# Kernel tuning notes

Measured on AMD Instinct MI355X. Metric: run time of the kernel, lower is better.

Reference implementation:

```python
import jax, jax.numpy as jnp
import numpy as np

Z, N, D_MODEL, HEADS = 2, 2048, 1024, 16
DK = D_MODEL // HEADS


def setup_inputs() -> dict:
    key = jax.random.key(0)
    ks = jax.random.split(key, 9)
    xavier = (6.0 / (DK + D_MODEL)) ** 0.5
    x = jax.random.normal(ks[0], (Z, N, D_MODEL), jnp.float32)
    mask = jax.random.randint(ks[1], (Z, N), 0, 2) > 0  # bool validity mask
    q_proj = jax.random.uniform(ks[2], (HEADS, D_MODEL, DK), jnp.float32, -xavier, xavier)
    k_proj = jax.random.uniform(ks[3], (HEADS, D_MODEL, DK), jnp.float32, -xavier, xavier)
    v_proj = jax.random.uniform(ks[4], (HEADS, D_MODEL, DK), jnp.float32, -xavier, xavier)
    q_bias = jnp.zeros((HEADS, DK), jnp.float32)
    k_bias = jnp.zeros((HEADS, DK), jnp.float32)
    v_bias = jnp.zeros((HEADS, DK), jnp.float32)
    lim = 1.0 / (D_MODEL ** 0.5)
    out_w = jax.random.uniform(ks[5], (D_MODEL, D_MODEL), jnp.float32, -lim, lim)  # torch Linear weight [out, in]
    return {"x": x, "mask": mask, "q_proj": q_proj, "k_proj": k_proj, "v_proj": v_proj,
            "q_bias": q_bias, "k_bias": k_bias, "v_bias": v_bias, "out_w": out_w}


def reference(x, mask, q_proj, k_proj, v_proj, q_bias, k_bias, v_bias, out_w):
    # Per-head QKV projections: [Z,N,Dm] x [H,Dm,Dk] -> [Z,H,N,Dk]
    Q = jnp.einsum('znd,hdk->zhnk', x, q_proj) + q_bias[None, :, None, :]
    K = jnp.einsum('znd,hdk->zhnk', x, k_proj) + k_bias[None, :, None, :]
    V = jnp.einsum('znd,hdk->zhnk', x, v_proj) + v_bias[None, :, None, :]
    scale = q_proj.shape[-1] ** -0.5
    # Dense equivalent of flash_attn_varlen over valid (unpadded) tokens:
    # mask invalid keys, softmax, then zero outputs at invalid query positions.
    scores = jnp.einsum('zhnk,zhmk->zhnm', Q, K) * scale
    neg = jnp.asarray(-1e9, scores.dtype)
    scores = jnp.where(mask[:, None, None, :], scores, neg)
    attn = jax.nn.softmax(scores, axis=-1)
    ctx = jnp.einsum('zhnm,zhmk->zhnk', attn, V)
    ctx = jnp.where(mask[:, None, :, None], ctx, jnp.zeros((), ctx.dtype))
    z, h, n, dk = ctx.shape
    out = ctx.transpose(0, 2, 1, 3).reshape(z, n, h * dk)  # [Z,N,Dm]
    return out @ out_w.T  # nn.Linear(d_model, d_model, bias=False)
```

## Files before the change

### kernel.cpp

```cpp
#include <hip/hip_runtime.h>
#include <stdint.h>

typedef __bf16 bf16_t;
typedef __bf16 bf16x8 __attribute__((ext_vector_type(8)));
typedef __bf16 bf16x4 __attribute__((ext_vector_type(4)));
typedef float f32x4 __attribute__((ext_vector_type(4)));

#define MFMA16(A, B, C) __builtin_amdgcn_mfma_f32_16x16x32_bf16(A, B, C, 0, 0, 0)

#if __has_builtin(__builtin_amdgcn_exp2f)
#define EXP2F(x) __builtin_amdgcn_exp2f(x)
#else
#define EXP2F(x) exp2f(x)
#endif

#define GLOAD_LDS16(g, l)                                                   \
  __builtin_amdgcn_global_load_lds(                                         \
      (const __attribute__((address_space(1))) void*)(g),                   \
      (__attribute__((address_space(3))) void*)(l), 16, 0, 0)

#define SL2E 0.18033688011112042f
#define VT_STRIDE 131072

__global__ __launch_bounds__(256) void convert_kernel(
    const float* __restrict__ x, const float* __restrict__ qw, const float* __restrict__ kw,
    const float* __restrict__ vw, const float* __restrict__ qb, const float* __restrict__ kb,
    const float* __restrict__ vb, const float* __restrict__ ow,
    bf16_t* __restrict__ xb, bf16_t* __restrict__ wqkv, bf16_t* __restrict__ wo,
    float* __restrict__ bias)
{
  const int64_t TOT = 4194304LL + 3145728LL + 1048576LL + 3072LL;
  for (int64_t idx = (int64_t)blockIdx.x * blockDim.x + threadIdx.x; idx < TOT;
       idx += (int64_t)gridDim.x * blockDim.x) {
    if (idx < 4194304) {
      xb[idx] = (bf16_t)x[idx];
    } else if (idx < 4194304 + 3145728) {
      int j = (int)(idx - 4194304);
      int nn = j >> 10, d = j & 1023;
      int sec = nn >> 10, hk = nn & 1023;
      int h = hk >> 6, k = hk & 63;
      const float* w = sec == 0 ? qw : (sec == 1 ? kw : vw);
      wqkv[j] = (bf16_t)w[(h * 1024 + d) * 64 + k];
    } else if (idx < 4194304 + 3145728 + 1048576) {
      int j = (int)(idx - (4194304 + 3145728));
      wo[j] = (bf16_t)ow[j];
    } else {
      int j = (int)(idx - (4194304 + 3145728 + 1048576));
      int sec = j >> 10, c = j & 1023;
      const float* b = sec == 0 ? qb : (sec == 1 ? kb : vb);
      bias[j] = b[c];
    }
  }
}

template <int MODE, int TM>
__global__ __launch_bounds__(256) void gemm_kernel(
    const bf16_t* __restrict__ A, const bf16_t* __restrict__ Bt, const float* __restrict__ bias,
    bf16_t* __restrict__ qout, bf16_t* __restrict__ kout, bf16_t* __restrict__ vtout,
    float* __restrict__ fout, int Ndim)
{
  const int Kdim = 1024;
  const int MT = TM / 32;
  __shared__ bf16_t As[TM * 64];
  __shared__ bf16_t Bs[128 * 64];
  const int tid = threadIdx.x;
  const int wave = tid >> 6, lane = tid & 63;
  const int l15 = lane & 15, quad = lane >> 4;
  const int wr = wave >> 1, wc = wave & 1;
  const int nb = Ndim >> 7;
  const int bm = (blockIdx.x / nb) * TM;
  const int bn = (blockIdx.x % nb) * 128;

  f32x4 acc[MT][4] = {};

  const int lr = lane >> 3;
  const int lc = (lane & 7) * 8;

  for (int kk = 0; kk < Kdim; kk += 64) {
    __syncthreads();
#pragma unroll
    for (int j = 0; j < MT; j++) {
      int r = wave * (TM / 4) + j * 8;
      GLOAD_LDS16(A + (int64_t)(bm + r + lr) * Kdim + kk + lc, &As[r * 64]);
    }
#pragma unroll
    for (int j = 0; j < 4; j++) {
      int r = wave * 32 + j * 8;
      GLOAD_LDS16(Bt + (int64_t)(bn + r + lr) * Kdim + kk + lc, &Bs[r * 64]);
    }
    __syncthreads();
#pragma unroll
    for (int kc = 0; kc < 2; kc++) {
      bf16x8 af[MT], bfr[4];
#pragma unroll
      for (int mt = 0; mt < MT; mt++)
        af[mt] = *(const bf16x8*)&As[(wr * (TM / 2) + mt * 16 + l15) * 64 + kc * 32 + quad * 8];
#pragma unroll
      for (int nt = 0; nt < 4; nt++)
        bfr[nt] = *(const bf16x8*)&Bs[(wc * 64 + nt * 16 + l15) * 64 + kc * 32 + quad * 8];
#pragma unroll
      for (int mt = 0; mt < MT; mt++)
#pragma unroll
        for (int nt = 0; nt < 4; nt++) acc[mt][nt] = MFMA16(af[mt], bfr[nt], acc[mt][nt]);
    }
  }

#pragma unroll
  for (int mt = 0; mt < MT; mt++) {
#pragma unroll
    for (int nt = 0; nt < 4; nt++) {
#pragma unroll
      for (int r = 0; r < 4; r++) {
        int row = bm + wr * (TM / 2) + mt * 16 + quad * 4 + r;
        int col = bn + wc * 64 + nt * 16 + l15;
        float v = acc[mt][nt][r];
        if (MODE == 0) {
          v += bias[col];
          int sec = col >> 10, hk = col & 1023;
          int hh = hk >> 6, dk = hk & 63;
          int z = row >> 11, n = row & 2047;
          int zh = z * 16 + hh;
          if (sec == 0) {
            qout[(((int64_t)zh * 2048 + n) << 6) + dk] = (bf16_t)(v * SL2E);
          } else if (sec == 1) {
            kout[(((int64_t)zh * 2048 + n) << 6) + dk] = (bf16_t)v;
          } else {
            vtout[(int64_t)zh * VT_STRIDE + dk * 2048 + n] = (bf16_t)v;
          }
        } else {
          fout[(int64_t)row * Ndim + col] = v;
        }
      }
    }
  }
}

__global__ __launch_bounds__(256, 2) void attn_kernel(
    const bf16_t* __restrict__ Q, const bf16_t* __restrict__ K, const bf16_t* __restrict__ Vt,
    const int* __restrict__ mask, bf16_t* __restrict__ ctx)
{
  __shared__ bf16_t Ks[2][64 * 72];
  __shared__ bf16_t Vs[2][64 * 72];
  __shared__ float Mkf[2048];
  __shared__ bf16_t Ps[4][32 * 72];

  const int tid = threadIdx.x;
  const int wave = tid >> 6, lane = tid & 63;
  const int l15 = lane & 15, quad = lane >> 4;
  const int bid = blockIdx.x;
  const int qt = bid & 15, zh = bid >> 4;
  const int z = zh >> 4, h = zh & 15;

  const bf16_t* Qb = Q + ((int64_t)zh * 2048 + qt * 128) * 64;
  const bf16_t* Kb = K + (int64_t)zh * 2048 * 64;
  const bf16_t* Vb = Vt + (int64_t)zh * VT_STRIDE;
  bf16_t* Psw = Ps[wave];

  const int srow = lane >> 3;
  const int scol = (lane & 7) * 8;

  bf16x8 qf[2][2];
#pragma unroll
  for (int s = 0; s < 2; s++) {
    qf[s][0] = *(const bf16x8*)&Qb[(wave * 32 + s * 16 + l15) * 64 + quad * 8];
    qf[s][1] = *(const bf16x8*)&Qb[(wave * 32 + s * 16 + l15) * 64 + 32 + quad * 8];
  }

  {
    const int4* mp = (const int4*)(mask + z * 2048);
    for (int i = tid; i < 512; i += 256) {
      int4 m4 = mp[i];
      float4 f;
      f.x = m4.x ? 0.f : -1e30f;
      f.y = m4.y ? 0.f : -1e30f;
      f.z = m4.z ? 0.f : -1e30f;
      f.w = m4.w ? 0.f : -1e30f;
      *(float4*)&Mkf[i * 4] = f;
    }
  }

  {
    uint4 kp[2], vp[2];
#pragma unroll
    for (int j = 0; j < 2; j++) {
      int r = wave * 16 + j * 8 + srow;
      kp[j] = *(const uint4*)&Kb[(int64_t)r * 64 + scol];
      vp[j] = *(const uint4*)&Vb[(int64_t)r * 2048 + scol];
    }
#pragma unroll
    for (int j = 0; j < 2; j++) {
      int r = wave * 16 + j * 8 + srow;
      *(uint4*)&Ks[0][r * 72 + scol] = kp[j];
      *(uint4*)&Vs[0][r * 72 + scol] = vp[j];
    }
  }
  __syncthreads();

  float l_run[2] = {0.f, 0.f};
  f32x4 o[2][4] = {};
  int cur = 0;

  for (int kt = 0; kt < 32; kt++) {
    uint4 kp[2], vp[2];
    if (kt < 31) {
#pragma unroll
      for (int j = 0; j < 2; j++) {
        int r = wave * 16 + j * 8 + srow;
        kp[j] = *(const uint4*)&Kb[(int64_t)((kt + 1) * 64 + r) * 64 + scol];
        vp[j] = *(const uint4*)&Vb[(int64_t)r * 2048 + (kt + 1) * 64 + scol];
      }
    }

    f32x4 minit[4];
    bf16x8 kf0[4], kf1[4];
#pragma unroll
    for (int mb = 0; mb < 4; mb++) {
      minit[mb] = *(const f32x4*)&Mkf[kt * 64 + mb * 16 + quad * 4];
      kf0[mb] = *(const bf16x8*)&Ks[cur][(mb * 16 + l15) * 72 + quad * 8];
      kf1[mb] = *(const bf16x8*)&Ks[cur][(mb * 16 + l15) * 72 + 32 + quad * 8];
    }

#pragma unroll
    for (int s = 0; s < 2; s++) {
      float rs = 0.f;
#pragma unroll
      for (int mb = 0; mb < 4; mb++) {
        f32x4 t = minit[mb];
        t = MFMA16(kf0[mb], qf[s][0], t);
        t = MFMA16(kf1[mb], qf[s][1], t);
        bf16x4 pk;
#pragma unroll
        for (int r = 0; r < 4; r++) {
          float p = EXP2F(t[r]);
          rs += p;
          pk[r] = (bf16_t)p;
        }
        *(bf16x4*)&Psw[(s * 16 + l15) * 72 + mb * 16 + quad * 4] = pk;
      }
      l_run[s] += rs;
    }

    bf16x8 p0[2], p1[2];
#pragma unroll
    for (int s = 0; s < 2; s++) {
      p0[s] = *(const bf16x8*)&Psw[(s * 16 + l15) * 72 + quad * 8];
      p1[s] = *(const bf16x8*)&Psw[(s * 16 + l15) * 72 + 32 + quad * 8];
    }

#pragma unroll
    for (int nb = 0; nb < 4; nb++) {
      bf16x8 v0 = *(const bf16x8*)&Vs[cur][(nb * 16 + l15) * 72 + quad * 8];
      bf16x8 v1 = *(const bf16x8*)&Vs[cur][(nb * 16 + l15) * 72 + 32 + quad * 8];
#pragma unroll
      for (int s = 0; s < 2; s++) {
        o[s][nb] = MFMA16(p0[s], v0, o[s][nb]);
        o[s][nb] = MFMA16(p1[s], v1, o[s][nb]);
      }
    }

    if (kt < 31) {
#pragma unroll
      for (int j = 0; j < 2; j++) {
        int r = wave * 16 + j * 8 + srow;
        *(uint4*)&Ks[cur ^ 1][r * 72 + scol] = kp[j];
        *(uint4*)&Vs[cur ^ 1][r * 72 + scol] = vp[j];
      }
    }
    __syncthreads();
    cur ^= 1;
  }

#pragma unroll
  for (int s = 0; s < 2; s++) {
    float l = l_run[s];
    l += __shfl_xor(l, 16);
    l += __shfl_xor(l, 32);
    float inv4[4];
#pragma unroll
    for (int r = 0; r < 4; r++) {
      int qrow = qt * 128 + wave * 32 + s * 16 + quad * 4 + r;
      float lv = __shfl(l, quad * 4 + r);
      int valid = mask[z * 2048 + qrow];
      inv4[r] = (valid && lv > 0.f) ? 1.0f / lv : 0.f;
    }
#pragma unroll
    for (int nb = 0; nb < 4; nb++) {
#pragma unroll
      for (int r = 0; r < 4; r++) {
        int qrow = qt * 128 + wave * 32 + s * 16 + quad * 4 + r;
        ctx[((int64_t)(z * 2048 + qrow)) * 1024 + h * 64 + nb * 16 + l15] =
            (bf16_t)(o[s][nb][r] * inv4[r]);
      }
    }
  }
}

extern "C" void kernel_launch(void* const* d_in, const int* in_sizes, int n_in,
                              void* d_out, int out_size, void* d_ws, size_t ws_size,
                              hipStream_t stream)
{
  (void)in_sizes; (void)n_in; (void)out_size; (void)ws_size;
  const float* x  = (const float*)d_in[0];
  const int* mask = (const int*)d_in[1];
  const float* qw = (const float*)d_in[2];
  const float* kw = (const float*)d_in[3];
  const float* vw = (const float*)d_in[4];
  const float* qb = (const float*)d_in[5];
  const float* kb = (const float*)d_in[6];
  const float* vb = (const float*)d_in[7];
  const float* ow = (const float*)d_in[8];
  float* out = (float*)d_out;

  bf16_t* xb   = (bf16_t*)d_ws;
  bf16_t* wqkv = xb + 4194304;
  bf16_t* wo   = wqkv + 3145728;
  float*  bias = (float*)(wo + 1048576);
  bf16_t* Qb   = (bf16_t*)(bias + 3072);
  bf16_t* Kb   = Qb + 4194304;
  bf16_t* Vtb  = Kb + 4194304;
  bf16_t* ctx  = Vtb + (int64_t)32 * VT_STRIDE;

  convert_kernel<<<4096, 256, 0, stream>>>(x, qw, kw, vw, qb, kb, vb, ow,
                                           xb, wqkv, wo, bias);
  gemm_kernel<0, 128><<<(4096 / 128) * (3072 / 128), 256, 0, stream>>>(
      xb, wqkv, bias, Qb, Kb, Vtb, nullptr, 3072);
  attn_kernel<<<2 * 16 * 16, 256, 0, stream>>>(Qb, Kb, Vtb, mask, ctx);
  gemm_kernel<1, 64><<<(4096 / 64) * (1024 / 128), 256, 0, stream>>>(
      ctx, wo, nullptr, nullptr, nullptr, nullptr, out, 1024);
}
```

Measured before the change: 238.3 us.

## Vectorize conversion, double-buffer GEMM loads, XCD-aware tiling, coalesce V transpose store

The conversion kernel now uses per-block roles: an LDS-tiled transpose for the QKV weights and vectorized float4-to-bf16x8 conversion for x and the output weight, replacing the scalar grid-stride loop. The GEMM gains a double-buffered LDS pipeline with explicit waitcnt/barrier so global-to-LDS loads overlap MFMA work. Block indices are remapped so that tiles sharing rows land on the same XCD, which targets better L2 reuse. The transposed V output is staged through LDS so it can be written with coalesced 16-byte stores. Together these target memory inefficiency in the preprocessing and projection stages, at the cost of more LDS use and hand-placed synchronization.

```diff
diff --git a/kernel.cpp b/kernel.cpp
--- a/kernel.cpp
+++ b/kernel.cpp
@@ -29,23 +29,49 @@
     bf16_t* __restrict__ xb, bf16_t* __restrict__ wqkv, bf16_t* __restrict__ wo,
     float* __restrict__ bias)
 {
-  const int64_t TOT = 4194304LL + 3145728LL + 1048576LL + 3072LL;
-  for (int64_t idx = (int64_t)blockIdx.x * blockDim.x + threadIdx.x; idx < TOT;
-       idx += (int64_t)gridDim.x * blockDim.x) {
-    if (idx < 4194304) {
-      xb[idx] = (bf16_t)x[idx];
-    } else if (idx < 4194304 + 3145728) {
-      int j = (int)(idx - 4194304);
-      int nn = j >> 10, d = j & 1023;
-      int sec = nn >> 10, hk = nn & 1023;
-      int h = hk >> 6, k = hk & 63;
-      const float* w = sec == 0 ? qw : (sec == 1 ? kw : vw);
-      wqkv[j] = (bf16_t)w[(h * 1024 + d) * 64 + k];
-    } else if (idx < 4194304 + 3145728 + 1048576) {
-      int j = (int)(idx - (4194304 + 3145728));
-      wo[j] = (bf16_t)ow[j];
-    } else {
-      int j = (int)(idx - (4194304 + 3145728 + 1048576));
+  const int bid = blockIdx.x, tid = threadIdx.x;
+  if (bid < 768) {
+    __shared__ float tile[64][65];
+    int sh = bid >> 4, db = bid & 15;
+    int sec = sh >> 4, h = sh & 15;
+    int d0 = db * 64;
+    const float* w = sec == 0 ? qw : (sec == 1 ? kw : vw);
+    int dd = tid >> 2, kk0 = (tid & 3) * 16;
+    const float* src = &w[((int64_t)h * 1024 + d0 + dd) * 64 + kk0];
+#pragma unroll
+    for (int j = 0; j < 4; j++) {
+      float4 v = *(const float4*)&src[j * 4];
+      tile[dd][kk0 + j * 4 + 0] = v.x;
+      tile[dd][kk0 + j * 4 + 1] = v.y;
+      tile[dd][kk0 + j * 4 + 2] = v.z;
+      tile[dd][kk0 + j * 4 + 3] = v.w;
+    }
+    __syncthreads();
+    int kk = tid >> 2, dd0 = (tid & 3) * 16;
+    bf16x8 o0, o1;
+#pragma unroll
+    for (int j = 0; j < 8; j++) o0[j] = (bf16_t)tile[dd0 + j][kk];
+#pragma unroll
+    for (int j = 0; j < 8; j++) o1[j] = (bf16_t)tile[dd0 + 8 + j][kk];
+    bf16_t* dst = &wqkv[(int64_t)(sh * 64 + kk) * 1024 + d0 + dd0];
+    *(bf16x8*)dst = o0;
+    *(bf16x8*)(dst + 8) = o1;
+  } else if (bid < 2816) {
+    int64_t base = ((int64_t)(bid - 768) * 256 + tid) * 8;
+    float4 a = *(const float4*)&x[base];
+    float4 b = *(const float4*)&x[base + 4];
+    bf16x8 o = {(bf16_t)a.x, (bf16_t)a.y, (bf16_t)a.z, (bf16_t)a.w,
+                (bf16_t)b.x, (bf16_t)b.y, (bf16_t)b.z, (bf16_t)b.w};
+    *(bf16x8*)&xb[base] = o;
+  } else if (bid < 3328) {
+    int64_t base = ((int64_t)(bid - 2816) * 256 + tid) * 8;
+    float4 a = *(const float4*)&ow[base];
+    float4 b = *(const float4*)&ow[base + 4];
+    bf16x8 o = {(bf16_t)a.x, (bf16_t)a.y, (bf16_t)a.z, (bf16_t)a.w,
+                (bf16_t)b.x, (bf16_t)b.y, (bf16_t)b.z, (bf16_t)b.w};
+    *(bf16x8*)&wo[base] = o;
+  } else {
+    for (int j = tid; j < 3072; j += 256) {
       int sec = j >> 10, c = j & 1023;
       const float* b = sec == 0 ? qb : (sec == 1 ? kb : vb);
       bias[j] = b[c];
@@ -61,48 +87,98 @@
 {
   const int Kdim = 1024;
   const int MT = TM / 32;
-  __shared__ bf16_t As[TM * 64];
-  __shared__ bf16_t Bs[128 * 64];
+  const int AS_SZ = TM * 64, BS_SZ = 128 * 64, BUF = AS_SZ + BS_SZ;
+  __shared__ bf16_t smem[2 * (TM * 64 + 128 * 64)];
+
   const int tid = threadIdx.x;
   const int wave = tid >> 6, lane = tid & 63;
   const int l15 = lane & 15, quad = lane >> 4;
   const int wr = wave >> 1, wc = wave & 1;
-  const int nb = Ndim >> 7;
-  const int bm = (blockIdx.x / nb) * TM;
-  const int bn = (blockIdx.x % nb) * 128;
+
+  const int MB = 4096 / TM;
+  const int GPX = MB / 8;
+  const int xcd = blockIdx.x & 7, j = blockIdx.x >> 3;
+  const int bm = (xcd * GPX + (j % GPX)) * TM;
+  const int bn = (j / GPX) * 128;
 
   f32x4 acc[MT][4] = {};
 
   const int lr = lane >> 3;
   const int lc = (lane & 7) * 8;
 
-  for (int kk = 0; kk < Kdim; kk += 64) {
-    __syncthreads();
-#pragma unroll
-    for (int j = 0; j < MT; j++) {
-      int r = wave * (TM / 4) + j * 8;
-      GLOAD_LDS16(A + (int64_t)(bm + r + lr) * Kdim + kk + lc, &As[r * 64]);
-    }
-#pragma unroll
-    for (int j = 0; j < 4; j++) {
-      int r = wave * 32 + j * 8;
-      GLOAD_LDS16(Bt + (int64_t)(bn + r + lr) * Kdim + kk + lc, &Bs[r * 64]);
-    }
-    __syncthreads();
+  auto stage = [&](int b, int kk) {
+    bf16_t* as = smem + b * BUF;
+    bf16_t* bs = as + AS_SZ;
+#pragma unroll
+    for (int jj = 0; jj < MT; jj++) {
+      int r = wave * (TM / 4) + jj * 8;
+      GLOAD_LDS16(A + (int64_t)(bm + r + lr) * Kdim + kk + lc, &as[r * 64]);
+    }
+#pragma unroll
+    for (int jj = 0; jj < 4; jj++) {
+      int r = wave * 32 + jj * 8;
+      GLOAD_LDS16(Bt + (int64_t)(bn + r + lr) * Kdim + kk + lc, &bs[r * 64]);
+    }
+  };
+
+  stage(0, 0);
+  for (int it = 0; it < 16; ++it) {
+    int cur = it & 1;
+    if (it < 15) {
+      asm volatile("s_waitcnt lgkmcnt(0)\n\ts_barrier" ::: "memory");
+      stage(cur ^ 1, (it + 1) * 64);
+      asm volatile("s_waitcnt vmcnt(%0)" ::"i"(MT + 4) : "memory");
+    } else {
+      asm volatile("s_waitcnt vmcnt(0)" ::: "memory");
+    }
+    asm volatile("s_barrier" ::: "memory");
+    const bf16_t* as = smem + cur * BUF;
+    const bf16_t* bs = as + AS_SZ;
 #pragma unroll
     for (int kc = 0; kc < 2; kc++) {
       bf16x8 af[MT], bfr[4];
 #pragma unroll
       for (int mt = 0; mt < MT; mt++)
-        af[mt] = *(const bf16x8*)&As[(wr * (TM / 2) + mt * 16 + l15) * 64 + kc * 32 + quad * 8];
+        af[mt] = *(const bf16x8*)&as[(wr * (TM / 2) + mt * 16 + l15) * 64 + kc * 32 + quad * 8];
 #pragma unroll
       for (int nt = 0; nt < 4; nt++)
-        bfr[nt] = *(const bf16x8*)&Bs[(wc * 64 + nt * 16 + l15) * 64 + kc * 32 + quad * 8];
+        bfr[nt] = *(const bf16x8*)&bs[(wc * 64 + nt * 16 + l15) * 64 + kc * 32 + quad * 8];
 #pragma unroll
       for (int mt = 0; mt < MT; mt++)
 #pragma unroll
         for (int nt = 0; nt < 4; nt++) acc[mt][nt] = MFMA16(af[mt], bfr[nt], acc[mt][nt]);
     }
+  }
+
+  if (MODE == 0 && bn >= 2048) {
+    __syncthreads();
+    bf16_t* Ct = smem;
+    const int CTS = 136;
+#pragma unroll
+    for (int mt = 0; mt < MT; mt++) {
+#pragma unroll
+      for (int nt = 0; nt < 4; nt++) {
+        int c = wc * 64 + nt * 16 + l15;
+        int rw = wr * (TM / 2) + mt * 16 + quad * 4;
+        bf16x4 pv;
+#pragma unroll
+        for (int r = 0; r < 4; r++) pv[r] = (bf16_t)(acc[mt][nt][r] + bias[bn + c]);
+        *(bf16x4*)&Ct[c * CTS + rw] = pv;
+      }
+    }
+    __syncthreads();
+    int z = bm >> 11, n0 = bm & 2047;
+    int colb = tid >> 4, nch = (tid & 15) * 8;
+#pragma unroll
+    for (int p = 0; p < 8; p++) {
+      int c = p * 16 + colb;
+      int hk = (bn + c) & 1023;
+      int hh = hk >> 6, dk = hk & 63;
+      int zh = z * 16 + hh;
+      bf16x8 vv = *(const bf16x8*)&Ct[c * CTS + nch];
+      *(bf16x8*)&vtout[(int64_t)zh * VT_STRIDE + dk * 2048 + n0 + nch] = vv;
+    }
+    return;
   }
 
 #pragma unroll
@@ -122,10 +198,8 @@
           int zh = z * 16 + hh;
           if (sec == 0) {
             qout[(((int64_t)zh * 2048 + n) << 6) + dk] = (bf16_t)(v * SL2E);
-          } else if (sec == 1) {
+          } else {
             kout[(((int64_t)zh * 2048 + n) << 6) + dk] = (bf16_t)v;
-          } else {
-            vtout[(int64_t)zh * VT_STRIDE + dk * 2048 + n] = (bf16_t)v;
           }
         } else {
           fout[(int64_t)row * Ndim + col] = v;
@@ -320,7 +394,7 @@
   bf16_t* Vtb  = Kb + 4194304;
   bf16_t* ctx  = Vtb + (int64_t)32 * VT_STRIDE;
 
-  convert_kernel<<<4096, 256, 0, stream>>>(x, qw, kw, vw, qb, kb, vb, ow,
+  convert_kernel<<<3329, 256, 0, stream>>>(x, qw, kw, vw, qb, kb, vb, ow,
                                            xb, wqkv, wo, bias);
   gemm_kernel<0, 128><<<(4096 / 128) * (3072 / 128), 256, 0, stream>>>(
       xb, wqkv, bias, Qb, Kb, Vtb, nullptr, 3072);
```

Measured after the change: 199.2 us. 16.4% less time.
